# Optimization experiments

Measured on AMD Instinct MI355X. Metric: run time of the kernel, lower is better.

The kernel has to match this reference:

```python
import jax, jax.numpy as jnp
import numpy as np

B, S, D, H = 4, 2048, 1024, 64  # batch, chunk_size, token_emb_dim, head_size

def setup_inputs() -> dict:
    key = jax.random.key(0)
    ks = jax.random.split(key, 6)
    sc = 0.02
    return {
        "x": jax.random.normal(ks[0], (B, S, D), dtype=jnp.float32),
        "Wq": jax.random.normal(ks[1], (D, H), dtype=jnp.float32) * sc,
        "Wk": jax.random.normal(ks[2], (D, H), dtype=jnp.float32) * sc,
        "Wv": jax.random.normal(ks[3], (D, H), dtype=jnp.float32) * sc,
        "Wproj": jax.random.normal(ks[4], (D, D), dtype=jnp.float32) * sc,
        "bproj": jax.random.normal(ks[5], (D,), dtype=jnp.float32) * sc,
        "n_heads": 16,
    }

def reference(x, Wq, Wk, Wv, Wproj, bproj, n_heads):
    # NOTE: the original torch module reuses ONE head instance n_heads times,
    # so every head produces the identical output. Compute once, tile.
    q = jnp.einsum('bsd,dh->bsh', x, Wq)
    k = jnp.einsum('bsd,dh->bsh', x, Wk)
    v = jnp.einsum('bsd,dh->bsh', x, Wv)
    scores = jnp.einsum('bqh,bkh->bqk', q, k) * (H ** -0.5)
    causal = jnp.tril(jnp.ones((S, S), dtype=bool))
    scores = jnp.where(causal[None, :, :], scores, -jnp.inf)
    attn = jax.nn.softmax(scores, axis=-1)
    ctx = jnp.einsum('bqk,bkh->bqh', attn, v)       # [B,S,H]
    out = jnp.tile(ctx, (1, 1, n_heads))            # concat of identical heads -> [B,S,D]
    return jnp.einsum('bsd,de->bse', out, Wproj) + bproj
```

## Files before the change

kernel.cpp:

```cpp
#include <hip/hip_runtime.h>
#include <hip/hip_bf16.h>
#include <math.h>

namespace {

constexpr int B = 4, S = 2048, D = 1024, H = 64, NH = 16;
constexpr int BS = B * S;
constexpr float SCALE2 = 0.125f * 1.4426950408889634f;
constexpr float M0 = 8.0f;

constexpr int AUNITS_PB = 272;
constexpr int AUNITS = AUNITS_PB * 4;

using f32x4 = __attribute__((ext_vector_type(4))) float;
using short8b = __attribute__((ext_vector_type(8))) short;

__device__ inline ushort f2bf(float f) {
    __hip_bfloat16 h = __float2bfloat16(f);
    return *reinterpret_cast<ushort*>(&h);
}
__device__ inline float bf2f(ushort u) {
    __hip_bfloat16 h = *reinterpret_cast<__hip_bfloat16*>(&u);
    return __bfloat162float(h);
}
__device__ inline int cum_units(int J) {
    return (J & 1) ? ((J + 1) * (J + 1) / 4) : (J * J / 4 + J / 2);
}

__global__ __launch_bounds__(256) void prep_kernel(const float* __restrict__ Wq,
                                                   const float* __restrict__ Wk,
                                                   const float* __restrict__ Wv,
                                                   const float* __restrict__ Wproj,
                                                   ushort* __restrict__ Wt,
                                                   ushort* __restrict__ Wpet) {
    const int bid = blockIdx.x;
    const int tid = threadIdx.x;
    if (bid < 768) {
        const int idx = bid * 256 + tid;
        const int n = idx >> 10, k = idx & 1023;
        const float* __restrict__ W = (n < 64) ? Wq : (n < 128) ? Wk : Wv;
        Wt[idx] = f2bf(W[k * 64 + (n & 63)]);
    } else {
        const int idx = (bid - 768) * 256 + tid;
        const int e = idx & 1023, h = idx >> 10;
        float s = 0.f;
#pragma unroll
        for (int t = 0; t < NH; ++t) s += Wproj[(t * H + h) * D + e];
        Wpet[e * 64 + h] = f2bf(s);
    }
}

__global__ __launch_bounds__(256) void qkv6_kernel(const float* __restrict__ x,
                                                   const ushort* __restrict__ Wt,
                                                   ushort* __restrict__ qb,
                                                   ushort* __restrict__ kb,
                                                   ushort* __restrict__ vb) {
    __shared__ ushort xs[16 * 128];
    __shared__ ushort wsm[192 * 128];
    const int tid = threadIdx.x;
    const int lane = tid & 63;
    const int li = lane & 15, lg = lane >> 4;
    const int wn = tid >> 6;
    const int row0 = blockIdx.x * 16;

    f32x4 acc[3];
#pragma unroll
    for (int t = 0; t < 3; ++t) acc[t] = (f32x4){0.f, 0.f, 0.f, 0.f};

    const int xrow = tid >> 4;
    const int xc4 = (tid & 15) * 4;

    const char* xsb = reinterpret_cast<const char*>(xs);
    const char* wsb = reinterpret_cast<const char*>(wsm);

    for (int k0 = 0; k0 < 1024; k0 += 128) {
        __syncthreads();
#pragma unroll
        for (int hh = 0; hh < 2; ++hh) {
            const float4 f = *reinterpret_cast<const float4*>(
                x + (size_t)(row0 + xrow) * 1024 + k0 + hh * 64 + xc4);
            ushort u[4] = {f2bf(f.x), f2bf(f.y), f2bf(f.z), f2bf(f.w)};
            int boff = xrow * 256 + (hh * 64 + xc4) * 2;
            boff ^= (xrow & 7) << 4;
            *reinterpret_cast<uint2*>(const_cast<char*>(xsb) + boff) =
                *reinterpret_cast<uint2*>(u);
        }
#pragma unroll
        for (int it = 0; it < 12; ++it) {
            const int cid = tid + it * 256;
            const int n = cid >> 4, kc = cid & 15;
            const int4 val = *reinterpret_cast<const int4*>(
                Wt + (size_t)n * 1024 + k0 + kc * 8);
            int boff = n * 256 + kc * 16;
            boff ^= (n & 7) << 4;
            *reinterpret_cast<int4*>(const_cast<char*>(wsb) + boff) = val;
        }
        __syncthreads();

        short8b a[4];
#pragma unroll
        for (int c2 = 0; c2 < 4; ++c2) {
            int aoff = li * 256 + c2 * 64 + lg * 16;
            aoff ^= (li & 7) << 4;
            a[c2] = *reinterpret_cast<const short8b*>(xsb + aoff);
        }
#pragma unroll
        for (int t = 0; t < 3; ++t) {
            const int n = wn * 48 + t * 16 + li;
            const int swz = (n & 7) << 4;
#pragma unroll
            for (int c2 = 0; c2 < 4; ++c2) {
                int boff = (n * 256 + c2 * 64 + lg * 16) ^ swz;
                const short8b bfrag = *reinterpret_cast<const short8b*>(wsb + boff);
                acc[t] = __builtin_amdgcn_mfma_f32_16x16x32_bf16(a[c2], bfrag, acc[t], 0, 0, 0);
            }
        }
    }

#pragma unroll
    for (int t = 0; t < 3; ++t) {
        const int col = wn * 48 + t * 16 + li;
        const int m = col >> 6, cc = col & 63;
        ushort* __restrict__ dst = (m == 0) ? qb : (m == 1) ? kb : vb;
        const float sc = (m == 0) ? SCALE2 : 1.f;
#pragma unroll
        for (int r = 0; r < 4; ++r) {
            const int gr = row0 + lg * 4 + r;
            dst[(size_t)gr * 64 + cc] = f2bf(acc[t][r] * sc);
        }
    }
}

__global__ __launch_bounds__(256) void attn_mfma4_kernel(const ushort* __restrict__ qb,
                                                         const ushort* __restrict__ kb16,
                                                         const ushort* __restrict__ vb16,
                                                         ushort* __restrict__ po,
                                                         float* __restrict__ pl) {
    __shared__ ushort ksm[128 * 64];
    __shared__ ushort vtm[64 * 128];
    __shared__ ushort plds[4][2][16 * 72];

    const int tid = threadIdx.x;
    const int lane = tid & 63;
    const int wave = tid >> 6;
    const int li = lane & 15, lg = lane >> 4;
    const int u = blockIdx.x;
    const int b = u & 3;
    const int ub = u >> 2;

    int J = (int)(2.f * sqrtf((float)ub + 0.5f));
    if (J > 31) J = 31;
    while (cum_units(J + 1) <= ub) ++J;
    while (cum_units(J) > ub) --J;
    const int c = ub - cum_units(J);
    const int key0 = c * 128;

    const ushort* qg = qb + (size_t)(b * S + J * 64 + wave * 16 + li) * 64 + lg * 8;
    const short8b aq0 = *reinterpret_cast<const short8b*>(qg);
    const short8b aq1 = *reinterpret_cast<const short8b*>(qg + 32);

    short8b bones;
#pragma unroll
    for (int i = 0; i < 8; ++i) bones[i] = (short)0x3F80;

    {
        const ushort* kg = kb16 + (size_t)(b * S + key0) * 64;
#pragma unroll
        for (int it = 0; it < 4; ++it) {
            const int f = tid + it * 256;
            const int key = f >> 3, hd8 = f & 7;
            const int4 val = *reinterpret_cast<const int4*>(kg + key * 64 + hd8 * 8);
            int byteoff = (key << 7) + (hd8 << 4);
            byteoff ^= (key & 7) << 4;
            *reinterpret_cast<int4*>(reinterpret_cast<char*>(ksm) + byteoff) = val;
        }
    }
    {
        const ushort* vg = vb16 + (size_t)(b * S + key0) * 64;
#pragma unroll
        for (int it = 0; it < 2; ++it) {
            const int item = tid + it * 256;
            const int kk = item >> 4;
            const int hq = item & 15;
            const uint2 a0 = *reinterpret_cast<const uint2*>(vg + (kk * 4 + 0) * 64 + hq * 4);
            const uint2 a1 = *reinterpret_cast<const uint2*>(vg + (kk * 4 + 1) * 64 + hq * 4);
            const uint2 a2 = *reinterpret_cast<const uint2*>(vg + (kk * 4 + 2) * 64 + hq * 4);
            const uint2 a3 = *reinterpret_cast<const uint2*>(vg + (kk * 4 + 3) * 64 + hq * 4);
#pragma unroll
            for (int i = 0; i < 4; ++i) {
                const uint s0 = (i < 2) ? a0.x : a0.y;
                const uint s1 = (i < 2) ? a1.x : a1.y;
                const uint s2 = (i < 2) ? a2.x : a2.y;
                const uint s3 = (i < 2) ? a3.x : a3.y;
                const uint sel = (i & 1) ? 0x07060302u : 0x05040100u;
                const uint w0 = __builtin_amdgcn_perm(s1, s0, sel);
                const uint w1 = __builtin_amdgcn_perm(s3, s2, sel);
                const int h = hq * 4 + i;
                int byteoff = (h << 8) + (kk << 3);
                byteoff ^= (h & 7) << 4;
                *reinterpret_cast<uint2*>(reinterpret_cast<char*>(vtm) + byteoff) =
                    make_uint2(w0, w1);
            }
        }
    }
    __syncthreads();

    f32x4 accs[8];
#pragma unroll
    for (int t = 0; t < 8; ++t) accs[t] = (f32x4){0.f, 0.f, 0.f, 0.f};
#pragma unroll
    for (int t = 0; t < 8; ++t) {
        const int key = t * 16 + li;
#pragma unroll
        for (int c2 = 0; c2 < 2; ++c2) {
            int byteoff = (key << 7) + (c2 << 6) + (lg << 4);
            byteoff ^= (key & 7) << 4;
            const short8b bk = *reinterpret_cast<const short8b*>(
                reinterpret_cast<const char*>(ksm) + byteoff);
            accs[t] = __builtin_amdgcn_mfma_f32_16x16x32_bf16(
                (c2 == 0) ? aq0 : aq1, bk, accs[t], 0, 0, 0);
        }
    }

    f32x4 oacc[4];
#pragma unroll
    for (int t = 0; t < 4; ++t) oacc[t] = (f32x4){0.f, 0.f, 0.f, 0.f};
    f32x4 lacc = (f32x4){0.f, 0.f, 0.f, 0.f};

#pragma unroll
    for (int half = 0; half < 2; ++half) {
#pragma unroll
        for (int tt = 0; tt < 4; ++tt) {
            const int t = half * 4 + tt;
            const int key = key0 + t * 16 + li;
#pragma unroll
            for (int r = 0; r < 4; ++r) {
                const int qrow = J * 64 + wave * 16 + lg * 4 + r;
                const float s = (key > qrow) ? -1e30f : accs[t][r];
                plds[wave][half][(lg * 4 + r) * 72 + tt * 16 + li] = f2bf(exp2f(s - M0));
            }
        }

        const char* pb = reinterpret_cast<const char*>(plds[wave][half]);
        const short8b ap0 = *reinterpret_cast<const short8b*>(pb + li * 144 + (lg << 4));
        const short8b ap1 = *reinterpret_cast<const short8b*>(pb + li * 144 + 64 + (lg << 4));
#pragma unroll
        for (int t = 0; t < 4; ++t) {
            const int h = t * 16 + li;
#pragma unroll
            for (int c2 = 0; c2 < 2; ++c2) {
                int byteoff = (h << 8) + (half << 7) + (c2 << 6) + (lg << 4);
                byteoff ^= (h & 7) << 4;
                const short8b bv = *reinterpret_cast<const short8b*>(
                    reinterpret_cast<const char*>(vtm) + byteoff);
                oacc[t] = __builtin_amdgcn_mfma_f32_16x16x32_bf16(
                    (c2 == 0) ? ap0 : ap1, bv, oacc[t], 0, 0, 0);
            }
        }
        lacc = __builtin_amdgcn_mfma_f32_16x16x32_bf16(ap0, bones, lacc, 0, 0, 0);
        lacc = __builtin_amdgcn_mfma_f32_16x16x32_bf16(ap1, bones, lacc, 0, 0, 0);
    }

    if (li == 0) {
#pragma unroll
        for (int r = 0; r < 4; ++r)
            pl[u * 64 + wave * 16 + lg * 4 + r] = lacc[r];
    }
#pragma unroll
    for (int t = 0; t < 4; ++t)
#pragma unroll
        for (int r = 0; r < 4; ++r)
            po[(size_t)u * 4096 + (wave * 16 + lg * 4 + r) * 64 + t * 16 + li] =
                f2bf(oacc[t][r]);
}

__global__ __launch_bounds__(256) void proj_fused_kernel(const ushort* __restrict__ po,
                                                         const float* __restrict__ pl,
                                                         const ushort* __restrict__ Wpet,
                                                         const float* __restrict__ bias,
                                                         float* __restrict__ out) {
    __shared__ ushort ctxs[16 * 64];
    const int tid = threadIdx.x;
    const int bid = blockIdx.x;
    const int b = bid >> 7, j = bid & 127;
    const int J = j >> 2;
    const int nc = (J + 2) >> 1;
    const int cumJ = cum_units(J);

    {
        const int qr = tid >> 4, hq = tid & 15;
        const int riu = (j & 3) * 16 + qr;
        float denom = 0.f;
        float acc[4] = {0.f, 0.f, 0.f, 0.f};
#pragma unroll
        for (int cc = 0; cc < 16; ++cc) {
            const int ccv = (cc < nc) ? cc : 0;
            const float w = (cc < nc) ? 1.f : 0.f;
            const int uu = (cumJ + ccv) * 4 + b;
            denom += w * pl[uu * 64 + riu];
            const uint2 v = *reinterpret_cast<const uint2*>(
                po + (size_t)uu * 4096 + riu * 64 + hq * 4);
            acc[0] += w * bf2f((ushort)(v.x & 0xffffu));
            acc[1] += w * bf2f((ushort)(v.x >> 16));
            acc[2] += w * bf2f((ushort)(v.y & 0xffffu));
            acc[3] += w * bf2f((ushort)(v.y >> 16));
        }
        const float inv = 1.f / denom;
        ushort uu4[4] = {f2bf(acc[0] * inv), f2bf(acc[1] * inv),
                         f2bf(acc[2] * inv), f2bf(acc[3] * inv)};
        int boff = qr * 128 + hq * 8;
        boff ^= (qr & 7) << 4;
        *reinterpret_cast<uint2*>(reinterpret_cast<char*>(ctxs) + boff) =
            *reinterpret_cast<uint2*>(uu4);
    }
    __syncthreads();

    const int lane = tid & 63;
    const int li = lane & 15, lg = lane >> 4;
    const int wave = tid >> 6;
    const int col0 = wave * 256;
    const int row0 = bid * 16;

    int aoff = li * 128 + lg * 16;
    aoff ^= (li & 7) << 4;
    const short8b a0 = *reinterpret_cast<const short8b*>(
        reinterpret_cast<const char*>(ctxs) + aoff);
    const short8b a1 = *reinterpret_cast<const short8b*>(
        reinterpret_cast<const char*>(ctxs) + (aoff ^ 64));

#pragma unroll
    for (int t = 0; t < 16; ++t) {
        const int col = col0 + t * 16 + li;
        const ushort* bg = Wpet + (size_t)col * 64 + lg * 8;
        const short8b b0 = *reinterpret_cast<const short8b*>(bg);
        const short8b b1 = *reinterpret_cast<const short8b*>(bg + 32);
        f32x4 acc = (f32x4){0.f, 0.f, 0.f, 0.f};
        acc = __builtin_amdgcn_mfma_f32_16x16x32_bf16(a0, b0, acc, 0, 0, 0);
        acc = __builtin_amdgcn_mfma_f32_16x16x32_bf16(a1, b1, acc, 0, 0, 0);
        const float bb = bias[col];
#pragma unroll
        for (int r = 0; r < 4; ++r)
            out[(size_t)(row0 + lg * 4 + r) * 1024 + col] = acc[r] + bb;
    }
}

}

extern "C" void kernel_launch(void* const* d_in, const int* in_sizes, int n_in,
                              void* d_out, int out_size, void* d_ws, size_t ws_size,
                              hipStream_t stream) {
    const float* x     = (const float*)d_in[0];
    const float* Wq    = (const float*)d_in[1];
    const float* Wk    = (const float*)d_in[2];
    const float* Wv    = (const float*)d_in[3];
    const float* Wproj = (const float*)d_in[4];
    const float* bproj = (const float*)d_in[5];
    float* out = (float*)d_out;

    const size_t BSH = (size_t)BS * H;
    ushort* qb   = (ushort*)d_ws;
    ushort* kb   = qb + BSH;
    ushort* vb   = kb + BSH;
    ushort* Wt   = vb + BSH;
    ushort* Wpet = Wt + 192 * 1024;
    ushort* po   = Wpet + 65536;
    float*  pl   = (float*)(po + (size_t)AUNITS * 4096);

    hipLaunchKernelGGL(prep_kernel, dim3(1024), dim3(256), 0, stream, Wq, Wk, Wv, Wproj, Wt, Wpet);
    hipLaunchKernelGGL(qkv6_kernel, dim3(BS / 16), dim3(256), 0, stream, x, Wt, qb, kb, vb);
    hipLaunchKernelGGL(attn_mfma4_kernel, dim3(AUNITS), dim3(256), 0, stream,
                       qb, kb, vb, po, pl);
    hipLaunchKernelGGL(proj_fused_kernel, dim3(512), dim3(256), 0, stream,
                       po, pl, Wpet, bproj, out);
}
```

Before: 50.29 us.

## Fuse split-K merge and output projection into attention via last-block atomic counter

```diff
diff --git a/kernel.cpp b/kernel.cpp
--- a/kernel.cpp
+++ b/kernel.cpp
@@ -32,9 +32,11 @@
                                                    const float* __restrict__ Wv,
                                                    const float* __restrict__ Wproj,
                                                    ushort* __restrict__ Wt,
-                                                   ushort* __restrict__ Wpet) {
+                                                   ushort* __restrict__ Wpet,
+                                                   int* __restrict__ cnt) {
     const int bid = blockIdx.x;
     const int tid = threadIdx.x;
+    if (bid == 0 && tid < 128) cnt[tid] = 0;
     if (bid < 768) {
         const int idx = bid * 256 + tid;
         const int n = idx >> 10, k = idx & 1023;
@@ -131,14 +133,19 @@
     }
 }
 
-__global__ __launch_bounds__(256) void attn_mfma4_kernel(const ushort* __restrict__ qb,
+__global__ __launch_bounds__(256) void attn_mfma5_kernel(const ushort* __restrict__ qb,
                                                          const ushort* __restrict__ kb16,
                                                          const ushort* __restrict__ vb16,
                                                          ushort* __restrict__ po,
-                                                         float* __restrict__ pl) {
+                                                         float* __restrict__ pl,
+                                                         const ushort* __restrict__ Wpet,
+                                                         const float* __restrict__ bias,
+                                                         float* __restrict__ out,
+                                                         int* __restrict__ cnt) {
     __shared__ ushort ksm[128 * 64];
     __shared__ ushort vtm[64 * 128];
     __shared__ ushort plds[4][2][16 * 72];
+    __shared__ int lastFlag;
 
     const int tid = threadIdx.x;
     const int lane = tid & 63;
@@ -272,75 +279,76 @@
         for (int r = 0; r < 4; ++r)
             po[(size_t)u * 4096 + (wave * 16 + lg * 4 + r) * 64 + t * 16 + li] =
                 f2bf(oacc[t][r]);
-}
-
-__global__ __launch_bounds__(256) void proj_fused_kernel(const ushort* __restrict__ po,
-                                                         const float* __restrict__ pl,
-                                                         const ushort* __restrict__ Wpet,
-                                                         const float* __restrict__ bias,
-                                                         float* __restrict__ out) {
-    __shared__ ushort ctxs[16 * 64];
-    const int tid = threadIdx.x;
-    const int bid = blockIdx.x;
-    const int b = bid >> 7, j = bid & 127;
-    const int J = j >> 2;
-    const int nc = (J + 2) >> 1;
+
+    const int ncg = (J + 2) >> 1;
+    __syncthreads();
+    if (tid == 0) {
+        __threadfence();
+        const int done = atomicAdd(&cnt[b * 32 + J], 1);
+        lastFlag = (done == ncg - 1) ? 1 : 0;
+    }
+    __syncthreads();
+    if (!lastFlag) return;
+    __threadfence();
+
     const int cumJ = cum_units(J);
-
-    {
-        const int qr = tid >> 4, hq = tid & 15;
-        const int riu = (j & 3) * 16 + qr;
-        float denom = 0.f;
-        float acc[4] = {0.f, 0.f, 0.f, 0.f};
-#pragma unroll
-        for (int cc = 0; cc < 16; ++cc) {
-            const int ccv = (cc < nc) ? cc : 0;
-            const float w = (cc < nc) ? 1.f : 0.f;
-            const int uu = (cumJ + ccv) * 4 + b;
-            denom += w * pl[uu * 64 + riu];
-            const uint2 v = *reinterpret_cast<const uint2*>(
-                po + (size_t)uu * 4096 + riu * 64 + hq * 4);
-            acc[0] += w * bf2f((ushort)(v.x & 0xffffu));
-            acc[1] += w * bf2f((ushort)(v.x >> 16));
-            acc[2] += w * bf2f((ushort)(v.y & 0xffffu));
-            acc[3] += w * bf2f((ushort)(v.y >> 16));
-        }
-        const float inv = 1.f / denom;
-        ushort uu4[4] = {f2bf(acc[0] * inv), f2bf(acc[1] * inv),
-                         f2bf(acc[2] * inv), f2bf(acc[3] * inv)};
-        int boff = qr * 128 + hq * 8;
-        boff ^= (qr & 7) << 4;
-        *reinterpret_cast<uint2*>(reinterpret_cast<char*>(ctxs) + boff) =
-            *reinterpret_cast<uint2*>(uu4);
-    }
-    __syncthreads();
-
-    const int lane = tid & 63;
-    const int li = lane & 15, lg = lane >> 4;
-    const int wave = tid >> 6;
-    const int col0 = wave * 256;
-    const int row0 = bid * 16;
-
-    int aoff = li * 128 + lg * 16;
-    aoff ^= (li & 7) << 4;
-    const short8b a0 = *reinterpret_cast<const short8b*>(
-        reinterpret_cast<const char*>(ctxs) + aoff);
-    const short8b a1 = *reinterpret_cast<const short8b*>(
-        reinterpret_cast<const char*>(ctxs) + (aoff ^ 64));
-
-#pragma unroll
-    for (int t = 0; t < 16; ++t) {
-        const int col = col0 + t * 16 + li;
-        const ushort* bg = Wpet + (size_t)col * 64 + lg * 8;
-        const short8b b0 = *reinterpret_cast<const short8b*>(bg);
-        const short8b b1 = *reinterpret_cast<const short8b*>(bg + 32);
-        f32x4 acc = (f32x4){0.f, 0.f, 0.f, 0.f};
-        acc = __builtin_amdgcn_mfma_f32_16x16x32_bf16(a0, b0, acc, 0, 0, 0);
-        acc = __builtin_amdgcn_mfma_f32_16x16x32_bf16(a1, b1, acc, 0, 0, 0);
-        const float bb = bias[col];
-#pragma unroll
-        for (int r = 0; r < 4; ++r)
-            out[(size_t)(row0 + lg * 4 + r) * 1024 + col] = acc[r] + bb;
+    ushort* ctxs = ksm;
+
+    for (int jj = 0; jj < 4; ++jj) {
+        const int j = J * 4 + jj;
+        __syncthreads();
+        {
+            const int qr = tid >> 4, hq = tid & 15;
+            const int riu = jj * 16 + qr;
+            float denom = 0.f;
+            float acc[4] = {0.f, 0.f, 0.f, 0.f};
+#pragma unroll
+            for (int cc = 0; cc < 16; ++cc) {
+                const int ccv = (cc < ncg) ? cc : 0;
+                const float w = (cc < ncg) ? 1.f : 0.f;
+                const int uu = (cumJ + ccv) * 4 + b;
+                denom += w * pl[uu * 64 + riu];
+                const uint2 v = *reinterpret_cast<const uint2*>(
+                    po + (size_t)uu * 4096 + riu * 64 + hq * 4);
+                acc[0] += w * bf2f((ushort)(v.x & 0xffffu));
+                acc[1] += w * bf2f((ushort)(v.x >> 16));
+                acc[2] += w * bf2f((ushort)(v.y & 0xffffu));
+                acc[3] += w * bf2f((ushort)(v.y >> 16));
+            }
+            const float inv = 1.f / denom;
+            ushort uu4[4] = {f2bf(acc[0] * inv), f2bf(acc[1] * inv),
+                             f2bf(acc[2] * inv), f2bf(acc[3] * inv)};
+            int boff = qr * 128 + hq * 8;
+            boff ^= (qr & 7) << 4;
+            *reinterpret_cast<uint2*>(reinterpret_cast<char*>(ctxs) + boff) =
+                *reinterpret_cast<uint2*>(uu4);
+        }
+        __syncthreads();
+
+        const int col0 = wave * 256;
+        const int row0 = (b * 128 + j) * 16;
+
+        int aoff = li * 128 + lg * 16;
+        aoff ^= (li & 7) << 4;
+        const short8b a0 = *reinterpret_cast<const short8b*>(
+            reinterpret_cast<const char*>(ctxs) + aoff);
+        const short8b a1 = *reinterpret_cast<const short8b*>(
+            reinterpret_cast<const char*>(ctxs) + (aoff ^ 64));
+
+#pragma unroll
+        for (int t = 0; t < 16; ++t) {
+            const int col = col0 + t * 16 + li;
+            const ushort* bg = Wpet + (size_t)col * 64 + lg * 8;
+            const short8b b0 = *reinterpret_cast<const short8b*>(bg);
+            const short8b b1 = *reinterpret_cast<const short8b*>(bg + 32);
+            f32x4 acc = (f32x4){0.f, 0.f, 0.f, 0.f};
+            acc = __builtin_amdgcn_mfma_f32_16x16x32_bf16(a0, b0, acc, 0, 0, 0);
+            acc = __builtin_amdgcn_mfma_f32_16x16x32_bf16(a1, b1, acc, 0, 0, 0);
+            const float bb = bias[col];
+#pragma unroll
+            for (int r = 0; r < 4; ++r)
+                out[(size_t)(row0 + lg * 4 + r) * 1024 + col] = acc[r] + bb;
+        }
     }
 }
 
@@ -365,11 +373,11 @@
     ushort* Wpet = Wt + 192 * 1024;
     ushort* po   = Wpet + 65536;
     float*  pl   = (float*)(po + (size_t)AUNITS * 4096);
-
-    hipLaunchKernelGGL(prep_kernel, dim3(1024), dim3(256), 0, stream, Wq, Wk, Wv, Wproj, Wt, Wpet);
+    int*    cnt  = (int*)(pl + AUNITS * 64);
+
+    hipLaunchKernelGGL(prep_kernel, dim3(1024), dim3(256), 0, stream,
+                       Wq, Wk, Wv, Wproj, Wt, Wpet, cnt);
     hipLaunchKernelGGL(qkv6_kernel, dim3(BS / 16), dim3(256), 0, stream, x, Wt, qb, kb, vb);
-    hipLaunchKernelGGL(attn_mfma4_kernel, dim3(AUNITS), dim3(256), 0, stream,
-                       qb, kb, vb, po, pl);
-    hipLaunchKernelGGL(proj_fused_kernel, dim3(512), dim3(256), 0, stream,
-                       po, pl, Wpet, bproj, out);
-}
+    hipLaunchKernelGGL(attn_mfma5_kernel, dim3(AUNITS), dim3(256), 0, stream,
+                       qb, kb, vb, po, pl, Wpet, bproj, out, cnt);
+}
```

Result: slower. 151.5 us (+201.2%).
